# Performance work log

Measured on AMD Instinct MI355X. Metric: run time of the kernel, lower is better.

Reference implementation:

```python
import jax, jax.numpy as jnp
import numpy as np

B, S, C = 1, 2048, 2048
H, D = 16, 128
FF = 8192
EPS = 1e-6


def _rms(x, w):
    return x * jax.lax.rsqrt(jnp.mean(x * x, axis=-1, keepdims=True) + EPS) * w


def _rope(x, cos, sin):
    # x: [B,S,H,D]; cos/sin: [S,D]
    x1, x2 = jnp.split(x, 2, axis=-1)
    rot = jnp.concatenate([-x2, x1], axis=-1)
    return x * cos[None, :, None, :] + rot * sin[None, :, None, :]


def setup_inputs() -> dict:
    key = jax.random.key(0)
    ks = jax.random.split(key, 12)
    # RoPE tables
    inv_freq = 1.0 / (10000.0 ** (jnp.arange(0, D, 2, dtype=jnp.float32) / D))
    freqs = jnp.arange(S, dtype=jnp.float32)[:, None] * inv_freq[None, :]
    emb = jnp.concatenate([freqs, freqs], axis=-1)  # [S,D]
    # causal additive mask
    causal = jnp.tril(jnp.ones((S, S), dtype=bool))
    mask = jnp.where(causal, 0.0, -1e9).astype(jnp.float32)[None, None]
    w = lambda k, shp: (jax.random.normal(k, shp, dtype=jnp.float32) * 0.02)
    return {
        "hidden_states": jax.random.normal(ks[0], (B, S, C), dtype=jnp.float32),
        "cos": jnp.cos(emb),
        "sin": jnp.sin(emb),
        "attention_mask": mask,
        "ln1_w": jnp.ones((C,), dtype=jnp.float32),
        "wq": w(ks[1], (C, C)),
        "wk": w(ks[2], (C, C)),
        "wv": w(ks[3], (C, C)),
        "wo": w(ks[4], (C, C)),
        "ln2_w": jnp.ones((C,), dtype=jnp.float32),
        "w_gate": w(ks[5], (FF, C)),
        "w_up": w(ks[6], (FF, C)),
        "w_down": w(ks[7], (C, FF)),
    }


def reference(hidden_states, cos, sin, attention_mask, ln1_w, wq, wk, wv, wo,
              ln2_w, w_gate, w_up, w_down):
    # --- input RMSNorm ---
    x = _rms(hidden_states, ln1_w)
    # --- W2 (Gaussian-kernel) attention ---
    q = (x @ wq.T).reshape(B, S, H, D)
    k = (x @ wk.T).reshape(B, S, H, D)
    v = (x @ wv.T).reshape(B, S, H, D)
    q = _rope(q, cos, sin).transpose(0, 2, 1, 3)  # [B,H,S,D]
    k = _rope(k, cos, sin).transpose(0, 2, 1, 3)
    v = v.transpose(0, 2, 1, 3)
    qk = jnp.einsum('bhid,bhjd->bhij', q, k)
    q2 = jnp.sum(q * q, axis=-1)  # [B,H,S]
    k2 = jnp.sum(k * k, axis=-1)
    dist2 = q2[..., :, None] - 2.0 * qk + k2[..., None, :]  # ||q-k||^2
    scores = -dist2 / (2.0 * np.sqrt(D).astype(np.float32)) + attention_mask
    attn = jax.nn.softmax(scores, axis=-1)
    ctx = jnp.einsum('bhij,bhjd->bhid', attn, v)
    attn_out = ctx.transpose(0, 2, 1, 3).reshape(B, S, C) @ wo.T
    h = hidden_states + attn_out
    # --- post-attn RMSNorm + SwiGLU FFN ---
    y = _rms(h, ln2_w)
    ffn = (jax.nn.silu(y @ w_gate.T) * (y @ w_up.T)) @ w_down.T
    return h + ffn
```

## Files before the change

### kernel.cpp

```cpp
#include <hip/hip_runtime.h>
#include <cstdint>
#include <cstddef>

typedef __bf16 bf16x8 __attribute__((ext_vector_type(8)));
typedef float f32x4 __attribute__((ext_vector_type(4)));

union V16 { uint4 u; bf16x8 b; unsigned short s[8]; };

__device__ __forceinline__ float b2f(unsigned short u) {
  unsigned int x = ((unsigned int)u) << 16;
  float f;
  __builtin_memcpy(&f, &x, 4);
  return f;
}
__device__ __forceinline__ unsigned short f2b(float f) {
  unsigned int u;
  __builtin_memcpy(&u, &f, 4);
  u = u + 0x7FFFu + ((u >> 16) & 1u);
  return (unsigned short)(u >> 16);
}

__device__ __forceinline__ f32x4 mfma16(bf16x8 a, bf16x8 b, f32x4 c) {
  return __builtin_amdgcn_mfma_f32_16x16x32_bf16(a, b, c, 0, 0, 0);
}

__device__ __forceinline__ void gld_lds16(const unsigned short* g, unsigned short* l) {
  __builtin_amdgcn_global_load_lds((__attribute__((address_space(1))) void*)g,
                                   (__attribute__((address_space(3))) void*)l,
                                   16, 0, 0);
}

__global__ __launch_bounds__(256) void cvt_all(const float* __restrict__ wq,
                                               const float* __restrict__ wk,
                                               const float* __restrict__ wv,
                                               const float* __restrict__ wo,
                                               const float* __restrict__ wg,
                                               const float* __restrict__ wu,
                                               const float* __restrict__ wd,
                                               unsigned short* __restrict__ dst) {
  const int b = blockIdx.x;
  const float* src;
  if (b < 16384) {
    const int w = b >> 12;
    src = (w == 0 ? wq : w == 1 ? wk : w == 2 ? wv : wo) + (size_t)(b & 4095) * 1024;
  } else if (b < 32768) {
    src = wg + (size_t)(b - 16384) * 1024;
  } else if (b < 49152) {
    src = wu + (size_t)(b - 32768) * 1024;
  } else {
    src = wd + (size_t)(b - 49152) * 1024;
  }
  const int o = threadIdx.x * 4;
  const float4 v = *(const float4*)(src + o);
  ushort4 r;
  r.x = f2b(v.x); r.y = f2b(v.y); r.z = f2b(v.z); r.w = f2b(v.w);
  *(ushort4*)(dst + (size_t)b * 1024 + o) = r;
}

__global__ __launch_bounds__(256) void rms_k(const float* __restrict__ xin,
                                             const float* __restrict__ wgt,
                                             unsigned short* __restrict__ out) {
  const int s = blockIdx.x;
  const int t = threadIdx.x;
  float vals[8];
  float ss = 0.f;
#pragma unroll
  for (int i = 0; i < 8; ++i) {
    const int c = t + i * 256;
    const float f = xin[(size_t)s * 2048 + c];
    vals[i] = f;
    ss += f * f;
  }
#pragma unroll
  for (int off = 32; off > 0; off >>= 1) ss += __shfl_xor(ss, off);
  __shared__ float red[4];
  if ((t & 63) == 0) red[t >> 6] = ss;
  __syncthreads();
  ss = red[0] + red[1] + red[2] + red[3];
  const float sc = rsqrtf(ss * (1.f / 2048.f) + 1e-6f);
#pragma unroll
  for (int i = 0; i < 8; ++i) {
    const int c = t + i * 256;
    out[(size_t)s * 2048 + c] = f2b(vals[i] * sc * wgt[c]);
  }
}

__global__ __launch_bounds__(256) void rope_qk(unsigned short* qb, unsigned short* kb,
                                               const float* __restrict__ cosb,
                                               const float* __restrict__ sinb,
                                               float* __restrict__ k2c) {
  const int idx = blockIdx.x * 256 + threadIdx.x;
  const int d = idx & 63;
  const int h = (idx >> 6) & 15;
  const int s = idx >> 10;
  const size_t base = (size_t)s * 2048 + h * 128;
  const int cb = s * 128;
  const float c1 = cosb[cb + d],      s1 = sinb[cb + d];
  const float c2 = cosb[cb + d + 64], s2 = sinb[cb + d + 64];
  {
    const float x1 = b2f(qb[base + d]), x2 = b2f(qb[base + d + 64]);
    qb[base + d]      = f2b(x1 * c1 - x2 * s1);
    qb[base + d + 64] = f2b(x2 * c2 + x1 * s2);
  }
  {
    const float x1 = b2f(kb[base + d]), x2 = b2f(kb[base + d + 64]);
    const float k1 = x1 * c1 - x2 * s1;
    const float k2 = x2 * c2 + x1 * s2;
    kb[base + d]      = f2b(k1);
    kb[base + d + 64] = f2b(k2);
    float ss = k1 * k1 + k2 * k2;
#pragma unroll
    for (int off = 32; off > 0; off >>= 1) ss += __shfl_xor(ss, off);
    if (d == 0) k2c[h * 2048 + s] = ss * 0.04419417382415922f;
  }
}

template <int EPI, int RT>
__global__ __launch_bounds__(256, 2) void gemm_nt(
    const unsigned short* __restrict__ A,
    const unsigned short* __restrict__ B0,
    const unsigned short* __restrict__ B1,
    const unsigned short* __restrict__ B2,
    unsigned short* C0, unsigned short* C1, unsigned short* C2,
    const float* auxf, float* Cf,
    int N, int K, int kstride) {
  constexpr int TM = RT * 32;
  constexpr int APASS = TM / 64;
  const unsigned short* B;
  unsigned short* C;
  size_t koff = 0;
  if constexpr (EPI == 0) {
    B = (blockIdx.z == 0) ? B0 : (blockIdx.z == 1 ? B1 : B2);
    C = (blockIdx.z == 0) ? C0 : (blockIdx.z == 1 ? C1 : C2);
  } else {
    B = B0;
    C = C0;
    if constexpr (EPI == 3) koff = (size_t)blockIdx.z * K;
  }

  const int m0 = blockIdx.y * TM;
  const int n0 = blockIdx.x * 128;
  const int t = threadIdx.x;
  const int lane = t & 63;
  const int w = t >> 6;
  const int quad = lane >> 4;
  const int l15 = lane & 15;
  const int wr = w >> 1;
  const int wc = w & 1;

  __shared__ __align__(16) unsigned short As[TM * 32];
  __shared__ __align__(16) unsigned short Bs[128 * 32];

  const f32x4 vzero = {0.f, 0.f, 0.f, 0.f};
  f32x4 acc[RT][4];
#pragma unroll
  for (int i = 0; i < RT; ++i)
#pragma unroll
    for (int j = 0; j < 4; ++j) acc[i][j] = vzero;

  const int srow = w * 16 + (lane >> 2);
  const int scol = (lane & 3) * 8;
  const unsigned short* Ag = A + (size_t)(m0 + srow) * kstride + scol + koff;
  const unsigned short* Bg = B + (size_t)(n0 + srow) * kstride + scol + koff;

  for (int k0 = 0; k0 < K; k0 += 32) {
#pragma unroll
    for (int p = 0; p < APASS; ++p)
      gld_lds16(Ag + (size_t)p * 64 * kstride + k0, As + p * 2048 + w * 512);
#pragma unroll
    for (int p = 0; p < 2; ++p)
      gld_lds16(Bg + (size_t)p * 64 * kstride + k0, Bs + p * 2048 + w * 512);
    __syncthreads();

    bf16x8 af[RT], bfr[4];
#pragma unroll
    for (int rt = 0; rt < RT; ++rt)
      af[rt] = *(const bf16x8*)&As[(wr * (RT * 16) + rt * 16 + l15) * 32 + quad * 8];
#pragma unroll
    for (int ct = 0; ct < 4; ++ct)
      bfr[ct] = *(const bf16x8*)&Bs[(wc * 64 + ct * 16 + l15) * 32 + quad * 8];
#pragma unroll
    for (int rt = 0; rt < RT; ++rt)
#pragma unroll
      for (int ct = 0; ct < 4; ++ct)
        acc[rt][ct] = mfma16(af[rt], bfr[ct], acc[rt][ct]);
    __syncthreads();
  }

  float* Cfz = Cf;
  if constexpr (EPI == 3)
    Cfz = Cf + (size_t)blockIdx.z * (size_t)gridDim.y * TM * N;

#pragma unroll
  for (int rt = 0; rt < RT; ++rt) {
#pragma unroll
    for (int ct = 0; ct < 4; ++ct) {
#pragma unroll
      for (int r = 0; r < 4; ++r) {
        const int m = m0 + wr * (RT * 16) + rt * 16 + quad * 4 + r;
        const int n = n0 + wc * 64 + ct * 16 + l15;
        const size_t idx = (size_t)m * N + n;
        const float a = acc[rt][ct][r];
        if constexpr (EPI == 0) {
          C[idx] = f2b(a);
        } else if constexpr (EPI == 1) {
          Cf[idx] = auxf[idx] + a;
        } else {
          Cfz[idx] = a;
        }
      }
    }
  }
}

__global__ __launch_bounds__(256, 2) void gemm_nt2(
    const unsigned short* __restrict__ A,
    const unsigned short* __restrict__ B0,
    const unsigned short* __restrict__ B1,
    unsigned short* __restrict__ C,
    int N, int K) {
  const int m0 = blockIdx.y * 128;
  const int n0 = blockIdx.x * 128;
  const int t = threadIdx.x;
  const int lane = t & 63;
  const int w = t >> 6;
  const int quad = lane >> 4;
  const int l15 = lane & 15;
  const int wr = w >> 1;
  const int wc = w & 1;

  __shared__ __align__(16) unsigned short As[128 * 32];
  __shared__ __align__(16) unsigned short B0s[128 * 32];
  __shared__ __align__(16) unsigned short B1s[128 * 32];

  const f32x4 vzero = {0.f, 0.f, 0.f, 0.f};
  f32x4 acc0[4][4], acc1[4][4];
#pragma unroll
  for (int i = 0; i < 4; ++i)
#pragma unroll
    for (int j = 0; j < 4; ++j) { acc0[i][j] = vzero; acc1[i][j] = vzero; }

  const int srow = w * 16 + (lane >> 2);
  const int scol = (lane & 3) * 8;
  const unsigned short* Ag  = A  + (size_t)(m0 + srow) * K + scol;
  const unsigned short* B0g = B0 + (size_t)(n0 + srow) * K + scol;
  const unsigned short* B1g = B1 + (size_t)(n0 + srow) * K + scol;

  for (int k0 = 0; k0 < K; k0 += 32) {
#pragma unroll
    for (int p = 0; p < 2; ++p) {
      gld_lds16(Ag  + (size_t)p * 64 * K + k0, As  + p * 2048 + w * 512);
      gld_lds16(B0g + (size_t)p * 64 * K + k0, B0s + p * 2048 + w * 512);
      gld_lds16(B1g + (size_t)p * 64 * K + k0, B1s + p * 2048 + w * 512);
    }
    __syncthreads();

    bf16x8 af[4], b0f[4], b1f[4];
#pragma unroll
    for (int rt = 0; rt < 4; ++rt)
      af[rt] = *(const bf16x8*)&As[(wr * 64 + rt * 16 + l15) * 32 + quad * 8];
#pragma unroll
    for (int ct = 0; ct < 4; ++ct) {
      b0f[ct] = *(const bf16x8*)&B0s[(wc * 64 + ct * 16 + l15) * 32 + quad * 8];
      b1f[ct] = *(const bf16x8*)&B1s[(wc * 64 + ct * 16 + l15) * 32 + quad * 8];
    }
#pragma unroll
    for (int rt = 0; rt < 4; ++rt)
#pragma unroll
      for (int ct = 0; ct < 4; ++ct) {
        acc0[rt][ct] = mfma16(af[rt], b0f[ct], acc0[rt][ct]);
        acc1[rt][ct] = mfma16(af[rt], b1f[ct], acc1[rt][ct]);
      }
    __syncthreads();
  }

#pragma unroll
  for (int rt = 0; rt < 4; ++rt) {
#pragma unroll
    for (int ct = 0; ct < 4; ++ct) {
#pragma unroll
      for (int r = 0; r < 4; ++r) {
        const int m = m0 + wr * 64 + rt * 16 + quad * 4 + r;
        const int n = n0 + wc * 64 + ct * 16 + l15;
        const float g = acc0[rt][ct][r];
        const float u = acc1[rt][ct][r];
        const float sg = g / (1.f + __expf(-g));
        C[(size_t)m * N + n] = f2b(sg * u);
      }
    }
  }
}

__global__ __launch_bounds__(256) void comb_k(const float* __restrict__ q0,
                                              const float* __restrict__ q1,
                                              const float* __restrict__ hf,
                                              float* __restrict__ out) {
  const int i = (blockIdx.x * 256 + threadIdx.x) * 4;
  const float4 a = *(const float4*)(q0 + i);
  const float4 b = *(const float4*)(q1 + i);
  const float4 c = *(const float4*)(hf + i);
  float4 r;
  r.x = a.x + b.x + c.x; r.y = a.y + b.y + c.y;
  r.z = a.z + b.z + c.z; r.w = a.w + b.w + c.w;
  *(float4*)(out + i) = r;
}

__global__ __launch_bounds__(256, 3) void flash_w2(
    const unsigned short* __restrict__ q,
    const unsigned short* __restrict__ kk,
    const unsigned short* __restrict__ v,
    const float* __restrict__ k2c,
    unsigned short* __restrict__ ctx) {
  constexpr int Cw = 2048;
  constexpr float TWOC = 0.08838834764831843f;
  const int h = blockIdx.y;
  const int i = (h >= 8) ? (31 - blockIdx.x) : blockIdx.x;
  const int i0 = i * 64;
  const int t = threadIdx.x;
  const int lane = t & 63;
  const int w = t >> 6;
  const int quad = lane >> 4;
  const int l15 = lane & 15;

  __shared__ __align__(16) unsigned short Ks[64 * 136];
  __shared__ __align__(16) unsigned short VTs[128 * 72];
  __shared__ __align__(16) unsigned short Ps[4][16 * 72];

  bf16x8 aq[4];
  {
    const unsigned short* qp = q + (size_t)(i0 + w * 16 + l15) * Cw + h * 128;
#pragma unroll
    for (int kt = 0; kt < 4; ++kt) {
      V16 u;
      u.u = *(const uint4*)(qp + kt * 32 + quad * 8);
      aq[kt] = u.b;
    }
  }

  const f32x4 vzero = {0.f, 0.f, 0.f, 0.f};
  f32x4 o[8];
#pragma unroll
  for (int nt = 0; nt < 8; ++nt) o[nt] = vzero;
  float mrow[4] = {-1e30f, -1e30f, -1e30f, -1e30f};
  float lrow[4] = {0.f, 0.f, 0.f, 0.f};

  const int njt = i + 1;
  const int jr = t >> 2;
  const int c0 = (t & 3) * 32;
  const int jlo = jr & 7;
  const int jhi = jr >> 3;
  for (int jt = 0; jt < njt; ++jt) {
    const int j0 = jt * 64;
    __syncthreads();
    {
      const unsigned short* kp = kk + (size_t)(j0 + jr) * Cw + h * 128 + c0;
      const unsigned short* vp = v + (size_t)(j0 + jr) * Cw + h * 128 + c0;
#pragma unroll
      for (int ii = 0; ii < 4; ++ii) {
        *(uint4*)&Ks[jr * 136 + c0 + ii * 8] = *(const uint4*)(kp + ii * 8);
        V16 vu;
        vu.u = *(const uint4*)(vp + ii * 8);
#pragma unroll
        for (int e = 0; e < 8; ++e) {
          const int dd = c0 + ii * 8 + e;
          const int gs = (jhi ^ (dd >> 4)) & 7;
          VTs[dd * 72 + (jlo | (gs << 3))] = vu.s[e];
        }
      }
    }
    __syncthreads();

    float k2v[4];
#pragma unroll
    for (int ct = 0; ct < 4; ++ct) k2v[ct] = k2c[h * 2048 + j0 + ct * 16 + l15];

    f32x4 sc[4];
#pragma unroll
    for (int ct = 0; ct < 4; ++ct) {
      f32x4 a = vzero;
#pragma unroll
      for (int kt = 0; kt < 4; ++kt) {
        V16 u;
        u.u = *(const uint4*)&Ks[(ct * 16 + l15) * 136 + kt * 32 + quad * 8];
        a = mfma16(aq[kt], u.b, a);
      }
      sc[ct] = a;
    }

    const bool diag = (jt == njt - 1);
#pragma unroll
    for (int ct = 0; ct < 4; ++ct) {
#pragma unroll
      for (int r = 0; r < 4; ++r) {
        float s = fmaf(TWOC, sc[ct][r], -k2v[ct]);
        if (diag) {
          const int gi = w * 16 + quad * 4 + r;
          const int gj = ct * 16 + l15;
          s = (gj <= gi) ? s : -1e30f;
        }
        sc[ct][r] = s;
      }
    }

    float al[4];
#pragma unroll
    for (int r = 0; r < 4; ++r) {
      float rm = fmaxf(fmaxf(sc[0][r], sc[1][r]), fmaxf(sc[2][r], sc[3][r]));
      rm = fmaxf(rm, __shfl_xor(rm, 1));
      rm = fmaxf(rm, __shfl_xor(rm, 2));
      rm = fmaxf(rm, __shfl_xor(rm, 4));
      rm = fmaxf(rm, __shfl_xor(rm, 8));
      const float mn = fmaxf(mrow[r], rm);
      al[r] = __expf(mrow[r] - mn);
      mrow[r] = mn;
      float ps = 0.f;
#pragma unroll
      for (int ct = 0; ct < 4; ++ct) {
        const float p = __expf(sc[ct][r] - mn);
        sc[ct][r] = p;
        ps += p;
      }
      ps += __shfl_xor(ps, 1);
      ps += __shfl_xor(ps, 2);
      ps += __shfl_xor(ps, 4);
      ps += __shfl_xor(ps, 8);
      lrow[r] = lrow[r] * al[r] + ps;
    }
#pragma unroll
    for (int nt = 0; nt < 8; ++nt)
#pragma unroll
      for (int r = 0; r < 4; ++r) o[nt][r] *= al[r];

#pragma unroll
    for (int ct = 0; ct < 4; ++ct)
#pragma unroll
      for (int r = 0; r < 4; ++r)
        Ps[w][(quad * 4 + r) * 72 + ct * 16 + l15] = f2b(sc[ct][r]);

#pragma unroll
    for (int kt2 = 0; kt2 < 2; ++kt2) {
      V16 pa;
      pa.u = *(const uint4*)&Ps[w][l15 * 72 + kt2 * 32 + quad * 8];
#pragma unroll
      for (int nt = 0; nt < 8; ++nt) {
        V16 vb;
        const int dd = nt * 16 + l15;
        const int gs = (kt2 * 4 + quad) ^ nt;
        vb.u = *(const uint4*)&VTs[dd * 72 + gs * 8];
        o[nt] = mfma16(pa.b, vb.b, o[nt]);
      }
    }
  }

  float invl[4];
#pragma unroll
  for (int r = 0; r < 4; ++r) invl[r] = 1.f / lrow[r];
#pragma unroll
  for (int nt = 0; nt < 8; ++nt) {
#pragma unroll
    for (int r = 0; r < 4; ++r) {
      const int gi = i0 + w * 16 + quad * 4 + r;
      ctx[(size_t)gi * Cw + h * 128 + nt * 16 + l15] = f2b(o[nt][r] * invl[r]);
    }
  }
}

extern "C" void kernel_launch(void* const* d_in, const int* in_sizes, int n_in,
                              void* d_out, int out_size, void* d_ws, size_t ws_size,
                              hipStream_t stream) {
  (void)in_sizes; (void)n_in; (void)out_size; (void)ws_size;
  const float* hid  = (const float*)d_in[0];
  const float* cosb = (const float*)d_in[1];
  const float* sinb = (const float*)d_in[2];
  const float* ln1w = (const float*)d_in[4];
  const float* wq   = (const float*)d_in[5];
  const float* wk   = (const float*)d_in[6];
  const float* wv   = (const float*)d_in[7];
  const float* wo   = (const float*)d_in[8];
  const float* ln2w = (const float*)d_in[9];
  const float* wg   = (const float*)d_in[10];
  const float* wu   = (const float*)d_in[11];
  const float* wd   = (const float*)d_in[12];
  float* outp = (float*)d_out;

  const size_t SC = (size_t)2048 * 2048;
  const size_t FC = (size_t)8192 * 2048;
  unsigned short* p = (unsigned short*)d_ws;
  unsigned short* wqb = p;  p += SC;
  unsigned short* wkb = p;  p += SC;
  unsigned short* wvb = p;  p += SC;
  unsigned short* wob = p;  p += SC;
  unsigned short* wgb = p;  p += FC;
  unsigned short* wub = p;  p += FC;
  unsigned short* wdb = p;  p += FC;
  unsigned short* xn  = p;  p += SC;
  unsigned short* qb  = p;  p += SC;
  unsigned short* kb  = p;  p += SC;
  unsigned short* vb  = p;  p += SC;
  unsigned short* ctxb = p; p += SC;
  float* hf = (float*)p;   p += 2 * SC;
  float* k2cb = (float*)p;
  unsigned short* yn = xn;
  unsigned short* gb = qb;
  float* qpart = (float*)wqb;

  cvt_all<<<65536, 256, 0, stream>>>(wq, wk, wv, wo, wg, wu, wd, wqb);

  rms_k<<<2048, 256, 0, stream>>>(hid, ln1w, xn);
  gemm_nt<0, 4><<<dim3(16, 16, 3), 256, 0, stream>>>(xn, wqb, wkb, wvb, qb, kb, vb,
                                                     nullptr, nullptr, 2048, 2048, 2048);
  rope_qk<<<8192, 256, 0, stream>>>(qb, kb, cosb, sinb, k2cb);
  flash_w2<<<dim3(32, 16), 256, 0, stream>>>(qb, kb, vb, k2cb, ctxb);
  gemm_nt<1, 2><<<dim3(16, 32, 1), 256, 0, stream>>>(ctxb, wob, wob, wob,
                                                     nullptr, nullptr, nullptr,
                                                     hid, hf, 2048, 2048, 2048);
  rms_k<<<2048, 256, 0, stream>>>(hf, ln2w, yn);
  gemm_nt2<<<dim3(64, 16), 256, 0, stream>>>(yn, wgb, wub, gb, 8192, 2048);
  gemm_nt<3, 4><<<dim3(16, 16, 2), 256, 0, stream>>>(gb, wdb, wdb, wdb,
                                                     nullptr, nullptr, nullptr,
                                                     nullptr, qpart, 2048, 4096, 8192);
  comb_k<<<4096, 256, 0, stream>>>(qpart, qpart + SC, hf, outp);
}
```

Baseline: 806.3 us.

## Replace QKV, gate/up and down GEMMs with pipelined 256x256 swizzled MFMA kernel

Adds a 512-thread gemm256 kernel that uses 256x256 output tiles, double-buffered direct-to-LDS loads with an XOR-swizzled LDS layout, and an explicit barrier/waitcnt schedule with MFMA priority raising. It also remaps workgroup IDs across XCD-style groups of eight. The kernel is used for the fused QKV projection (one 6144-wide GEMM), the fused gate/up projection (one 16384-wide GEMM followed by a separate SiLU-multiply kernel), and a 4-way split-K down projection reduced by a new combine kernel. The aim is to raise data reuse and MFMA utilisation in the dominant GEMMs. In exchange, the SiLU is no longer fused into the GEMM epilogue, which adds an extra pass over the intermediate, and the split-K writes and reads more fp32 partials.

```diff
diff --git a/kernel.cpp b/kernel.cpp
--- a/kernel.cpp
+++ b/kernel.cpp
@@ -213,96 +213,206 @@
   }
 }
 
-__global__ __launch_bounds__(256, 2) void gemm_nt2(
+#define BARRIER() asm volatile("s_barrier" ::: "memory")
+#define WAITVM(N) asm volatile("s_waitcnt vmcnt(" #N ")" ::: "memory")
+#define WAITLG()                                           \
+  do {                                                     \
+    asm volatile("s_waitcnt lgkmcnt(0)" ::: "memory");     \
+    __builtin_amdgcn_sched_barrier(0);                     \
+  } while (0)
+
+#define LOADA(APT, MQ)                                                         \
+  _Pragma("unroll") for (int j = 0; j < 4; ++j)                                \
+  _Pragma("unroll") for (int ks = 0; ks < 2; ++ks)                             \
+      afr[j][ks] = *(const bf16x8*)((APT) + ((MQ) * 64 + j * 16 + l15) * 64 +  \
+                                    (ks ? ko1 : ko0));
+
+#define LOADB(BPT, NQ)                                                         \
+  _Pragma("unroll") for (int jn = 0; jn < 2; ++jn)                             \
+  _Pragma("unroll") for (int ks = 0; ks < 2; ++ks)                             \
+      bfr[(NQ) * 2 + jn][ks] =                                                 \
+          *(const bf16x8*)((BPT) + ((NQ) * 32 + jn * 16 + l15) * 64 +          \
+                           (ks ? ko1 : ko0));
+
+#define MFMAQ(MQ, NQ)                                                          \
+  do {                                                                         \
+    __builtin_amdgcn_s_setprio(1);                                             \
+    _Pragma("unroll") for (int j = 0; j < 4; ++j)                              \
+    _Pragma("unroll") for (int jn = 0; jn < 2; ++jn)                           \
+    _Pragma("unroll") for (int ks = 0; ks < 2; ++ks)                           \
+        acc[(MQ) * 4 + j][(NQ) * 2 + jn] =                                     \
+            mfma16(afr[j][ks], bfr[(NQ) * 2 + jn][ks],                         \
+                   acc[(MQ) * 4 + j][(NQ) * 2 + jn]);                          \
+    __builtin_amdgcn_s_setprio(0);                                             \
+  } while (0)
+
+#define STAGE8(DA, DB)                                                         \
+  do {                                                                         \
+    _Pragma("unroll") for (int h = 0; h < 2; ++h)                              \
+    _Pragma("unroll") for (int i = 0; i < 2; ++i) {                            \
+      gld_lds16(sAg + (size_t)(h * 128 + i * 64) * kstr,                       \
+                (DA) + h * 8192 + i * 4096 + w * 512);                         \
+      gld_lds16(sBg + (size_t)(h * 128 + i * 64) * kstr,                       \
+                (DB) + h * 8192 + i * 4096 + w * 512);                         \
+    }                                                                          \
+    sAg += 64;                                                                 \
+    sBg += 64;                                                                 \
+  } while (0)
+
+#define TILEGRP(APT, BPT, STG, WTB)                                            \
+  do {                                                                         \
+    LOADA(APT, 0);                                                             \
+    LOADB(BPT, 0);                                                             \
+    BARRIER(); WAITLG(); MFMAQ(0, 0); BARRIER();                               \
+    LOADB(BPT, 1);                                                             \
+    BARRIER(); WAITLG(); MFMAQ(0, 1); BARRIER();                               \
+    LOADA(APT, 1);                                                             \
+    BARRIER(); WAITLG(); MFMAQ(1, 0); BARRIER();                               \
+    STG;                                                                       \
+    BARRIER(); MFMAQ(1, 1); WTB; BARRIER();                                    \
+  } while (0)
+
+template <int EPI>
+__global__ __launch_bounds__(512, 2) void gemm256(
     const unsigned short* __restrict__ A,
-    const unsigned short* __restrict__ B0,
-    const unsigned short* __restrict__ B1,
-    unsigned short* __restrict__ C,
-    int N, int K) {
-  const int m0 = blockIdx.y * 128;
-  const int n0 = blockIdx.x * 128;
+    const unsigned short* __restrict__ B,
+    unsigned short* __restrict__ C0,
+    unsigned short* __restrict__ C1,
+    unsigned short* __restrict__ C2,
+    float* __restrict__ Cf,
+    int N, int kstr, int Ktiles) {
+  const int gx = gridDim.x, gy = gridDim.y;
+  const int nwg = gx * gy * gridDim.z;
+  const int orig = blockIdx.x + gx * (blockIdx.y + gy * blockIdx.z);
+  const int s = ((nwg & 7) == 0) ? ((orig & 7) * (nwg >> 3) + (orig >> 3)) : orig;
+  const int bx = s % gx;
+  const int sq = s / gx;
+  const int by = sq % gy;
+  const int bz = sq / gy;
+
+  const int m0 = by * 256, n0 = bx * 256;
+  const size_t koff = (size_t)bz * ((size_t)Ktiles * 64);
+
   const int t = threadIdx.x;
   const int lane = t & 63;
   const int w = t >> 6;
   const int quad = lane >> 4;
   const int l15 = lane & 15;
-  const int wr = w >> 1;
-  const int wc = w & 1;
-
-  __shared__ __align__(16) unsigned short As[128 * 32];
-  __shared__ __align__(16) unsigned short B0s[128 * 32];
-  __shared__ __align__(16) unsigned short B1s[128 * 32];
+  const int wr = w >> 2;
+  const int wc = w & 3;
+
+  __shared__ __align__(16) unsigned short As[2][2][8192];
+  __shared__ __align__(16) unsigned short Bs[2][2][8192];
 
   const f32x4 vzero = {0.f, 0.f, 0.f, 0.f};
-  f32x4 acc0[4][4], acc1[4][4];
-#pragma unroll
-  for (int i = 0; i < 4; ++i)
-#pragma unroll
-    for (int j = 0; j < 4; ++j) { acc0[i][j] = vzero; acc1[i][j] = vzero; }
-
-  const int srow = w * 16 + (lane >> 2);
-  const int scol = (lane & 3) * 8;
-  const unsigned short* Ag  = A  + (size_t)(m0 + srow) * K + scol;
-  const unsigned short* B0g = B0 + (size_t)(n0 + srow) * K + scol;
-  const unsigned short* B1g = B1 + (size_t)(n0 + srow) * K + scol;
-
-  for (int k0 = 0; k0 < K; k0 += 32) {
-#pragma unroll
-    for (int p = 0; p < 2; ++p) {
-      gld_lds16(Ag  + (size_t)p * 64 * K + k0, As  + p * 2048 + w * 512);
-      gld_lds16(B0g + (size_t)p * 64 * K + k0, B0s + p * 2048 + w * 512);
-      gld_lds16(B1g + (size_t)p * 64 * K + k0, B1s + p * 2048 + w * 512);
-    }
-    __syncthreads();
-
-    bf16x8 af[4], b0f[4], b1f[4];
-#pragma unroll
-    for (int rt = 0; rt < 4; ++rt)
-      af[rt] = *(const bf16x8*)&As[(wr * 64 + rt * 16 + l15) * 32 + quad * 8];
-#pragma unroll
-    for (int ct = 0; ct < 4; ++ct) {
-      b0f[ct] = *(const bf16x8*)&B0s[(wc * 64 + ct * 16 + l15) * 32 + quad * 8];
-      b1f[ct] = *(const bf16x8*)&B1s[(wc * 64 + ct * 16 + l15) * 32 + quad * 8];
-    }
-#pragma unroll
-    for (int rt = 0; rt < 4; ++rt)
-#pragma unroll
-      for (int ct = 0; ct < 4; ++ct) {
-        acc0[rt][ct] = mfma16(af[rt], b0f[ct], acc0[rt][ct]);
-        acc1[rt][ct] = mfma16(af[rt], b1f[ct], acc1[rt][ct]);
-      }
-    __syncthreads();
-  }
-
-#pragma unroll
-  for (int rt = 0; rt < 4; ++rt) {
-#pragma unroll
-    for (int ct = 0; ct < 4; ++ct) {
-#pragma unroll
-      for (int r = 0; r < 4; ++r) {
-        const int m = m0 + wr * 64 + rt * 16 + quad * 4 + r;
-        const int n = n0 + wc * 64 + ct * 16 + l15;
-        const float g = acc0[rt][ct][r];
-        const float u = acc1[rt][ct][r];
-        const float sg = g / (1.f + __expf(-g));
-        C[(size_t)m * N + n] = f2b(sg * u);
-      }
-    }
-  }
-}
-
-__global__ __launch_bounds__(256) void comb_k(const float* __restrict__ q0,
-                                              const float* __restrict__ q1,
-                                              const float* __restrict__ hf,
-                                              float* __restrict__ out) {
-  const int i = (blockIdx.x * 256 + threadIdx.x) * 4;
-  const float4 a = *(const float4*)(q0 + i);
-  const float4 b = *(const float4*)(q1 + i);
-  const float4 c = *(const float4*)(hf + i);
-  float4 r;
-  r.x = a.x + b.x + c.x; r.y = a.y + b.y + c.y;
-  r.z = a.z + b.z + c.z; r.w = a.w + b.w + c.w;
-  *(float4*)(out + i) = r;
+  f32x4 acc[8][4];
+#pragma unroll
+  for (int i = 0; i < 8; ++i)
+#pragma unroll
+    for (int j = 0; j < 4; ++j) acc[i][j] = vzero;
+
+  bf16x8 afr[4][2], bfr[4][2];
+
+  const int lr = lane >> 3;
+  const int lc = ((lane & 7) ^ lr) * 8;
+  const unsigned short* sAg = A + (size_t)(m0 + w * 8 + lr) * kstr + koff + lc;
+  const unsigned short* sBg = B + (size_t)(n0 + w * 8 + lr) * kstr + koff + lc;
+
+  unsigned short* Asb0 = &As[0][0][0];
+  unsigned short* Asb1 = &As[1][0][0];
+  unsigned short* Bsb0 = &Bs[0][0][0];
+  unsigned short* Bsb1 = &Bs[1][0][0];
+  const unsigned short* Aw0 = &As[0][wr][0];
+  const unsigned short* Aw1 = &As[1][wr][0];
+  const unsigned short* Bw0 = &Bs[0][wc >> 1][0] + (wc & 1) * 4096;
+  const unsigned short* Bw1 = &Bs[1][wc >> 1][0] + (wc & 1) * 4096;
+
+  const int ax = (l15 & 7) * 8;
+  const int ko0 = (quad * 8) ^ ax;
+  const int ko1 = (32 + quad * 8) ^ ax;
+
+  STAGE8(Asb0, Bsb0);
+  STAGE8(Asb1, Bsb1);
+  WAITVM(8);
+  BARRIER();
+
+  const int nIter = (Ktiles >> 1) - 1;
+  for (int it = 0; it < nIter; ++it) {
+    TILEGRP(Aw0, Bw0, STAGE8(Asb0, Bsb0), WAITVM(8));
+    TILEGRP(Aw1, Bw1, STAGE8(Asb1, Bsb1), WAITVM(8));
+  }
+  TILEGRP(Aw0, Bw0, (void)0, WAITVM(0));
+  TILEGRP(Aw1, Bw1, (void)0, (void)0);
+
+  if constexpr (EPI == 2) {
+    const size_t MN = (size_t)gy * 256 * N;
+    float* Cp = Cf + (size_t)bz * MN;
+#pragma unroll
+    for (int mf = 0; mf < 8; ++mf) {
+      const int m = m0 + wr * 128 + mf * 16 + quad * 4;
+#pragma unroll
+      for (int nf = 0; nf < 4; ++nf) {
+        const int n = n0 + wc * 64 + nf * 16 + l15;
+#pragma unroll
+        for (int r = 0; r < 4; ++r) Cp[(size_t)(m + r) * N + n] = acc[mf][nf][r];
+      }
+    }
+  } else {
+    unsigned short* Cp;
+    int nb;
+    constexpr int ldc = (EPI == 0) ? 8192 : 2048;
+    if constexpr (EPI == 0) {
+      Cp = (n0 < 8192) ? C0 : C1;
+      nb = n0 & 8191;
+    } else {
+      const int wsel = n0 >> 11;
+      Cp = wsel == 0 ? C0 : (wsel == 1 ? C1 : C2);
+      nb = n0 & 2047;
+    }
+#pragma unroll
+    for (int mf = 0; mf < 8; ++mf) {
+      const int m = m0 + wr * 128 + mf * 16 + quad * 4;
+#pragma unroll
+      for (int nf = 0; nf < 4; ++nf) {
+        const int n = nb + wc * 64 + nf * 16 + l15;
+#pragma unroll
+        for (int r = 0; r < 4; ++r)
+          Cp[(size_t)(m + r) * ldc + n] = f2b(acc[mf][nf][r]);
+      }
+    }
+  }
+}
+
+__global__ __launch_bounds__(256) void silu_k(unsigned short* __restrict__ g,
+                                              const unsigned short* __restrict__ u) {
+  const size_t i = ((size_t)blockIdx.x * 256 + threadIdx.x) * 8;
+  V16 gv, uv, ov;
+  gv.u = *(const uint4*)(g + i);
+  uv.u = *(const uint4*)(u + i);
+#pragma unroll
+  for (int e = 0; e < 8; ++e) {
+    const float gf = b2f(gv.s[e]);
+    const float uf = b2f(uv.s[e]);
+    ov.s[e] = f2b(gf / (1.f + __expf(-gf)) * uf);
+  }
+  *(uint4*)(g + i) = ov.u;
+}
+
+__global__ __launch_bounds__(256) void comb4(const float* __restrict__ p,
+                                             const float* __restrict__ hf,
+                                             float* __restrict__ out) {
+  const size_t i = ((size_t)blockIdx.x * 256 + threadIdx.x) * 4;
+  const size_t MN = (size_t)2048 * 2048;
+  float4 a = *(const float4*)(p + i);
+  const float4 b = *(const float4*)(p + MN + i);
+  const float4 c = *(const float4*)(p + 2 * MN + i);
+  const float4 d = *(const float4*)(p + 3 * MN + i);
+  const float4 h = *(const float4*)(hf + i);
+  a.x += b.x + c.x + d.x + h.x;
+  a.y += b.y + c.y + d.y + h.y;
+  a.z += b.z + c.z + d.z + h.z;
+  a.w += b.w + c.w + d.w + h.w;
+  *(float4*)(out + i) = a;
 }
 
 __global__ __launch_bounds__(256, 3) void flash_w2(
@@ -501,23 +611,25 @@
   float* hf = (float*)p;   p += 2 * SC;
   float* k2cb = (float*)p;
   unsigned short* yn = xn;
-  unsigned short* gb = qb;
-  float* qpart = (float*)wqb;
+  unsigned short* gate = wqb;
+  unsigned short* upb  = qb;
+  float* pd = (float*)wgb;
 
   cvt_all<<<65536, 256, 0, stream>>>(wq, wk, wv, wo, wg, wu, wd, wqb);
 
   rms_k<<<2048, 256, 0, stream>>>(hid, ln1w, xn);
-  gemm_nt<0, 4><<<dim3(16, 16, 3), 256, 0, stream>>>(xn, wqb, wkb, wvb, qb, kb, vb,
-                                                     nullptr, nullptr, 2048, 2048, 2048);
+  gemm256<1><<<dim3(24, 8, 1), 512, 0, stream>>>(xn, wqb, qb, kb, vb, nullptr,
+                                                 6144, 2048, 32);
   rope_qk<<<8192, 256, 0, stream>>>(qb, kb, cosb, sinb, k2cb);
   flash_w2<<<dim3(32, 16), 256, 0, stream>>>(qb, kb, vb, k2cb, ctxb);
   gemm_nt<1, 2><<<dim3(16, 32, 1), 256, 0, stream>>>(ctxb, wob, wob, wob,
                                                      nullptr, nullptr, nullptr,
                                                      hid, hf, 2048, 2048, 2048);
   rms_k<<<2048, 256, 0, stream>>>(hf, ln2w, yn);
-  gemm_nt2<<<dim3(64, 16), 256, 0, stream>>>(yn, wgb, wub, gb, 8192, 2048);
-  gemm_nt<3, 4><<<dim3(16, 16, 2), 256, 0, stream>>>(gb, wdb, wdb, wdb,
-                                                     nullptr, nullptr, nullptr,
-                                                     nullptr, qpart, 2048, 4096, 8192);
-  comb_k<<<4096, 256, 0, stream>>>(qpart, qpart + SC, hf, outp);
-}
+  gemm256<0><<<dim3(64, 8, 1), 512, 0, stream>>>(yn, wgb, gate, upb, nullptr, nullptr,
+                                                 16384, 2048, 32);
+  silu_k<<<8192, 256, 0, stream>>>(gate, upb);
+  gemm256<2><<<dim3(8, 8, 4), 512, 0, stream>>>(gate, wdb, nullptr, nullptr, nullptr,
+                                                pd, 2048, 8192, 32);
+  comb4<<<4096, 256, 0, stream>>>(pd, hf, outp);
+}
```

New measurement: 825.6 us. +2.4%, slower.
